# Optimization experiments

Measured on AMD Instinct MI355X. Metric: run time of the kernel, lower is better.

Reference implementation:

```python
import jax, jax.numpy as jnp
import numpy as np

N = 50000     # nodes
E = 400000    # nnz per hop matrix
K1 = 4        # K + 1 hops (K = 3)
D = 1280      # in_dim (pad_features target_dim)
H = 256       # hidden_dim


def setup_inputs() -> dict:
    key = jax.random.key(0)
    k0, k1, k2, k3, k4, k5 = jax.random.split(key, 6)
    X = jax.random.normal(k0, (N, D), dtype=jnp.float32)
    rows = jax.random.randint(k1, (K1, E), 0, N, dtype=jnp.int32)
    cols = jax.random.randint(k2, (K1, E), 0, N, dtype=jnp.int32)
    vals = jax.random.uniform(k3, (K1, E), dtype=jnp.float32)
    W = jax.random.normal(k4, (K1, D, H), dtype=jnp.float32) * 0.02
    b = jax.random.normal(k5, (K1, H), dtype=jnp.float32) * 0.02
    alpha = jnp.ones((1,), dtype=jnp.float32) * 0.25  # PReLU default init
    return {"X": X, "rows": rows, "cols": cols, "vals": vals,
            "W": W, "b": b, "alpha": alpha}


def _spmm(rows_k, cols_k, vals_k, X):
    # sparse A_k @ X: gather source rows, scale by edge values, scatter-add to dest rows
    return jax.ops.segment_sum(vals_k[:, None] * X[cols_k], rows_k, num_segments=N)


def reference(X, rows, cols, vals, W, b, alpha):
    out = jnp.zeros((N, H), dtype=X.dtype)
    for k in range(K1):  # small fixed hop count, structurally distinct matrices
        tmp = _spmm(rows[k], cols[k], vals[k], X)       # [N, D]
        out = out + tmp @ W[k] + b[k]                    # [N, H]
    # PReLU with single shared alpha
    return jnp.where(out >= 0, out, alpha * out)
```

## Files before the change

kernel.cpp:

```cpp
#include <hip/hip_runtime.h>
#include <hip/hip_bf16.h>
#include <stdint.h>

#define N_NODES 50000
#define E_EDGES 400000
#define K1H 4
#define D_IN 1280
#define H_OUT 256
#define NTOT 1024
#define MP 50176
#define MTILES 392
#define CAP 128

typedef float f32x4 __attribute__((ext_vector_type(4)));
typedef short s16x8 __attribute__((ext_vector_type(8)));

#define GLOBAL_AS __attribute__((address_space(1)))
#define LDS_AS __attribute__((address_space(3)))

__device__ __forceinline__ void g2lds16(const void* g, void* l) {
    __builtin_amdgcn_global_load_lds((const GLOBAL_AS uint32_t*)g,
                                     (LDS_AS uint32_t*)l, 16, 0, 0);
}

__device__ __forceinline__ ushort f2bf(float x) {
    uint32_t u = __float_as_uint(x);
    uint32_t r = u + 0x7FFFu + ((u >> 16) & 1u);
    return (ushort)(r >> 16);
}
__device__ __forceinline__ float bf2f(ushort u) {
    return __uint_as_float(((uint32_t)u) << 16);
}

__global__ void cvtX_kernel(const float* __restrict__ X, ushort* __restrict__ Xb) {
    int i = (blockIdx.x * 256 + threadIdx.x) * 4;
    ushort4 o;
    if (i < N_NODES * D_IN) {
        const float4 v = *(const float4*)(X + i);
        o.x = f2bf(v.x); o.y = f2bf(v.y); o.z = f2bf(v.z); o.w = f2bf(v.w);
    } else {
        o.x = 0; o.y = 0; o.z = 0; o.w = 0;
    }
    *(ushort4*)(Xb + i) = o;
}

__global__ void cvtW_kernel(const float* __restrict__ W, ushort* __restrict__ WbT) {
    int o = blockIdx.x * 256 + threadIdx.x;
    if (o >= NTOT * D_IN) return;
    int n = o / D_IN, d = o - n * D_IN;
    int k = n >> 8, h = n & 255;
    WbT[o] = f2bf(W[(k * D_IN + d) * H_OUT + h]);
}

__global__ void scatter_kernel(const int* __restrict__ rows, const int* __restrict__ cols,
                               const float* __restrict__ vals, int* __restrict__ cnt,
                               int2* __restrict__ edges) {
    int i = blockIdx.x * 256 + threadIdx.x;
    if (i >= K1H * E_EDGES) return;
    int k = i / E_EDGES;
    int r = rows[i];
    int pos = atomicAdd(&cnt[r], 1);
    if (pos < CAP)
        edges[(size_t)r * CAP + pos] =
            make_int2((cols[i] << 10) | (k << 8), __float_as_int(vals[i]));
}

__global__ void __launch_bounds__(256)
gemm_kernel(const ushort* __restrict__ Xb, const ushort* __restrict__ WbT,
            ushort* __restrict__ Yb) {
    __shared__ ushort lA[128 * 64];
    __shared__ ushort lB[128 * 64];
    const int bid = blockIdx.x;
    const int xcd = bid & 7, j = bid >> 3;
    const int rt = xcd + ((j >> 3) << 3);
    const int ct = j & 7;
    const int rowBase = rt * 128;
    const int colBase = ct * 128;
    const int t = threadIdx.x;
    const int w = t >> 6, lane = t & 63;
    const int quad = lane >> 4, l16 = lane & 15;
    const int wm = w >> 1, wn = w & 1;

    f32x4 acc[4][4] = {};

    int gaA[4], gaB[4];
    #pragma unroll
    for (int i = 0; i < 4; ++i) {
        const int c = t + 256 * i;
        const int row = c >> 3, kcs = (c & 7) ^ (row & 7);
        gaA[i] = (rowBase + row) * D_IN + kcs * 8;
        gaB[i] = (colBase + row) * D_IN + kcs * 8;
    }

    for (int kt = 0; kt < D_IN / 64; ++kt) {
        const int ko = kt * 64;
        #pragma unroll
        for (int i = 0; i < 4; ++i) {
            g2lds16(Xb + gaA[i] + ko, &lA[(t + 256 * i) * 8]);
            g2lds16(WbT + gaB[i] + ko, &lB[(t + 256 * i) * 8]);
        }
        __syncthreads();

        #pragma unroll
        for (int ks = 0; ks < 2; ++ks) {
            s16x8 af[4], bf[4];
            #pragma unroll
            for (int mt = 0; mt < 4; ++mt) {
                const int m = wm * 64 + mt * 16 + l16;
                af[mt] = *(const s16x8*)&lA[(m * 8 + ((ks * 4 + quad) ^ (m & 7))) * 8];
            }
            #pragma unroll
            for (int nt = 0; nt < 4; ++nt) {
                const int n = wn * 64 + nt * 16 + l16;
                bf[nt] = *(const s16x8*)&lB[(n * 8 + ((ks * 4 + quad) ^ (n & 7))) * 8];
            }
            #pragma unroll
            for (int mt = 0; mt < 4; ++mt)
                #pragma unroll
                for (int nt = 0; nt < 4; ++nt)
                    acc[mt][nt] = __builtin_amdgcn_mfma_f32_16x16x32_bf16(
                        af[mt], bf[nt], acc[mt][nt], 0, 0, 0);
        }
        __syncthreads();
    }

    #pragma unroll
    for (int mt = 0; mt < 4; ++mt) {
        #pragma unroll
        for (int nt = 0; nt < 4; ++nt) {
            const int rr = rowBase + wm * 64 + mt * 16 + quad * 4;
            const int cc = colBase + wn * 64 + nt * 16 + l16;
            #pragma unroll
            for (int r = 0; r < 4; ++r)
                Yb[(rr + r) * NTOT + cc] = f2bf(acc[mt][nt][r]);
        }
    }
}

__global__ void __launch_bounds__(256)
spmm_kernel(const int2* __restrict__ edges, const int* __restrict__ cnt,
            const ushort* __restrict__ Yb, const float* __restrict__ b,
            const float* __restrict__ alpha, float* __restrict__ out) {
    const int wid = threadIdx.x >> 6, lane = threadIdx.x & 63;
    const int row = blockIdx.x * 4 + wid;
    const int h0 = lane * 4;

    float4 acc = make_float4(0.f, 0.f, 0.f, 0.f);
    #pragma unroll
    for (int k = 0; k < K1H; ++k) {
        const float4 bb = *(const float4*)(b + k * H_OUT + h0);
        acc.x += bb.x; acc.y += bb.y; acc.z += bb.z; acc.w += bb.w;
    }

    const int2* eb = edges + (size_t)row * CAP;
    int e = cnt[row]; if (e > CAP) e = CAP;
    int j = 0;
    for (; j + 4 <= e; j += 4) {
        const int2 e0 = eb[j], e1 = eb[j + 1], e2 = eb[j + 2], e3 = eb[j + 3];
        const ushort4 y0 = *(const ushort4*)(Yb + e0.x + h0);
        const ushort4 y1 = *(const ushort4*)(Yb + e1.x + h0);
        const ushort4 y2 = *(const ushort4*)(Yb + e2.x + h0);
        const ushort4 y3 = *(const ushort4*)(Yb + e3.x + h0);
        const float v0 = __int_as_float(e0.y), v1 = __int_as_float(e1.y);
        const float v2 = __int_as_float(e2.y), v3 = __int_as_float(e3.y);
        acc.x += v0 * bf2f(y0.x) + v1 * bf2f(y1.x) + v2 * bf2f(y2.x) + v3 * bf2f(y3.x);
        acc.y += v0 * bf2f(y0.y) + v1 * bf2f(y1.y) + v2 * bf2f(y2.y) + v3 * bf2f(y3.y);
        acc.z += v0 * bf2f(y0.z) + v1 * bf2f(y1.z) + v2 * bf2f(y2.z) + v3 * bf2f(y3.z);
        acc.w += v0 * bf2f(y0.w) + v1 * bf2f(y1.w) + v2 * bf2f(y2.w) + v3 * bf2f(y3.w);
    }
    for (; j < e; ++j) {
        const int2 ed = eb[j];
        const float v = __int_as_float(ed.y);
        const ushort4 y = *(const ushort4*)(Yb + ed.x + h0);
        acc.x += v * bf2f(y.x);
        acc.y += v * bf2f(y.y);
        acc.z += v * bf2f(y.z);
        acc.w += v * bf2f(y.w);
    }

    const float a = alpha[0];
    float4 o;
    o.x = acc.x >= 0.f ? acc.x : a * acc.x;
    o.y = acc.y >= 0.f ? acc.y : a * acc.y;
    o.z = acc.z >= 0.f ? acc.z : a * acc.z;
    o.w = acc.w >= 0.f ? acc.w : a * acc.w;
    *(float4*)(out + row * H_OUT + h0) = o;
}

static inline size_t align256(size_t x) { return (x + 255) & ~(size_t)255; }

extern "C" void kernel_launch(void* const* d_in, const int* in_sizes, int n_in,
                              void* d_out, int out_size, void* d_ws, size_t ws_size,
                              hipStream_t stream) {
    const float* X     = (const float*)d_in[0];
    const int*   rows  = (const int*)d_in[1];
    const int*   cols  = (const int*)d_in[2];
    const float* vals  = (const float*)d_in[3];
    const float* W     = (const float*)d_in[4];
    const float* b     = (const float*)d_in[5];
    const float* alpha = (const float*)d_in[6];
    float* out = (float*)d_out;

    char* ws = (char*)d_ws;
    size_t off = 0;
    ushort* Xb  = (ushort*)(ws + off); off = align256(off + (size_t)MP * D_IN * 2);
    ushort* WbT = (ushort*)(ws + off); off = align256(off + (size_t)NTOT * D_IN * 2);
    ushort* Yb  = (ushort*)(ws + off); off = align256(off + (size_t)MP * NTOT * 2);
    int* cnt    = (int*)(ws + off);    off = align256(off + (size_t)N_NODES * 4);
    int2* edges = (int2*)(ws + off);   off = align256(off + (size_t)N_NODES * CAP * 8);

    hipMemsetAsync(cnt, 0, (size_t)N_NODES * 4, stream);

    cvtX_kernel<<<MP * D_IN / 4 / 256, 256, 0, stream>>>(X, Xb);
    cvtW_kernel<<<(NTOT * D_IN + 255) / 256, 256, 0, stream>>>(W, WbT);
    scatter_kernel<<<(K1H * E_EDGES + 255) / 256, 256, 0, stream>>>(rows, cols, vals, cnt, edges);
    gemm_kernel<<<MTILES * 8, 256, 0, stream>>>(Xb, WbT, Yb);
    spmm_kernel<<<N_NODES / 4, 256, 0, stream>>>(edges, cnt, Yb, b, alpha, out);
}
```

Measured before the change: 781.9 us.

## Rewrite GEMM as 256x256-tile, 8-wave, double-buffered LDS pipeline

Reworks the bf16 GEMM to use 256x256 output tiles computed by 512 threads, with double-buffered LDS and a hand-scheduled loop. The loop interleaves global-to-LDS staging of the next K slice with MFMA work on the current one, using explicit vmcnt/lgkmcnt waits, barriers and setprio. Larger tiles raise arithmetic intensity per byte loaded, and the overlap aims to hide load latency. In exchange it uses 128KB of LDS and many more registers, and the hand-written wait counts are fragile.

```diff
diff --git a/kernel.cpp b/kernel.cpp
--- a/kernel.cpp
+++ b/kernel.cpp
@@ -9,7 +9,6 @@
 #define H_OUT 256
 #define NTOT 1024
 #define MP 50176
-#define MTILES 392
 #define CAP 128
 
 typedef float f32x4 __attribute__((ext_vector_type(4)));
@@ -65,77 +64,124 @@
             make_int2((cols[i] << 10) | (k << 8), __float_as_int(vals[i]));
 }
 
-__global__ void __launch_bounds__(256)
+#define BARR() __builtin_amdgcn_s_barrier()
+#define LGKM0() { asm volatile("s_waitcnt lgkmcnt(0)" ::: "memory"); \
+                  __builtin_amdgcn_sched_barrier(0); }
+#define VMC(N) asm volatile("s_waitcnt vmcnt(" #N ")" ::: "memory")
+
+__global__ void __launch_bounds__(512, 2)
 gemm_kernel(const ushort* __restrict__ Xb, const ushort* __restrict__ WbT,
             ushort* __restrict__ Yb) {
-    __shared__ ushort lA[128 * 64];
-    __shared__ ushort lB[128 * 64];
+    __shared__ ushort lds[2][2][256 * 64];
+
     const int bid = blockIdx.x;
     const int xcd = bid & 7, j = bid >> 3;
-    const int rt = xcd + ((j >> 3) << 3);
-    const int ct = j & 7;
-    const int rowBase = rt * 128;
-    const int colBase = ct * 128;
+    const int j2 = xcd * 98 + j;
+    const int rt = j2 >> 2, ct = j2 & 3;
+    const int rowBase = rt * 256, colBase = ct * 256;
     const int t = threadIdx.x;
     const int w = t >> 6, lane = t & 63;
     const int quad = lane >> 4, l16 = lane & 15;
-    const int wm = w >> 1, wn = w & 1;
-
-    f32x4 acc[4][4] = {};
-
-    int gaA[4], gaB[4];
+    const int wm = w >> 2, wn = w & 3;
+
+    f32x4 acc[8][4] = {};
+    s16x8 af[4][2];
+    s16x8 bfr[2][2][2];
+
+    const int kcg = (t & 7) ^ ((t >> 3) & 7);
+    const ushort* pA = Xb + (rowBase + (t >> 3)) * D_IN + kcg * 8;
+    const ushort* pB = WbT + (colBase + (t >> 3) + wm * 32) * D_IN + kcg * 8;
+
+#define STAGE_A(BUF, G, KT) { _Pragma("unroll") \
+    for (int r = 0; r < 2; ++r) \
+        g2lds16(pA + (r * 128 + (G) * 64) * D_IN + (KT) * 64, \
+                &lds[BUF][0][(t + (G) * 512 + r * 1024) * 8]); }
+#define STAGE_B(BUF, G, KT) { _Pragma("unroll") \
+    for (int r = 0; r < 2; ++r) \
+        g2lds16(pB + (r * 128 + (G) * 32) * D_IN + (KT) * 64, \
+                &lds[BUF][1][(t + wm * 256 + (G) * 256 + r * 1024) * 8]); }
+#define LDA_F(BUF, MH) { _Pragma("unroll") \
+    for (int mt = 0; mt < 4; ++mt) { \
+        const int m = wm * 128 + (MH) * 64 + mt * 16 + l16; \
+        _Pragma("unroll") for (int ks = 0; ks < 2; ++ks) \
+            af[mt][ks] = *(const s16x8*)&lds[BUF][0][(m * 8 + ((ks * 4 + quad) ^ (l16 & 7))) * 8]; } }
+#define LDB_F(BUF, NH) { _Pragma("unroll") \
+    for (int nt = 0; nt < 2; ++nt) { \
+        const int n = wn * 64 + (NH) * 32 + nt * 16 + l16; \
+        _Pragma("unroll") for (int ks = 0; ks < 2; ++ks) \
+            bfr[NH][nt][ks] = *(const s16x8*)&lds[BUF][1][(n * 8 + ((ks * 4 + quad) ^ (l16 & 7))) * 8]; } }
+#define MMA_Q(MH, NH) { __builtin_amdgcn_s_setprio(1); \
+    _Pragma("unroll") for (int mt = 0; mt < 4; ++mt) \
+        _Pragma("unroll") for (int nt = 0; nt < 2; ++nt) \
+            _Pragma("unroll") for (int ks = 0; ks < 2; ++ks) \
+                acc[(MH) * 4 + mt][(NH) * 2 + nt] = \
+                    __builtin_amdgcn_mfma_f32_16x16x32_bf16(af[mt][ks], bfr[NH][nt][ks], \
+                        acc[(MH) * 4 + mt][(NH) * 2 + nt], 0, 0, 0); \
+    __builtin_amdgcn_s_setprio(0); }
+
+    STAGE_A(0, 0, 0); STAGE_B(0, 0, 0); STAGE_A(0, 1, 0); STAGE_B(0, 1, 0);
+    STAGE_A(1, 0, 1); STAGE_B(1, 0, 1);
+    VMC(8);
+    BARR();
+
+#pragma unroll 1
+    for (int i = 0; i < 9; ++i) {
+        const int kt0 = 2 * i;
+        LDA_F(0, 0); LDB_F(0, 0); STAGE_A(1, 1, kt0 + 1); VMC(6);
+        BARR(); LGKM0(); MMA_Q(0, 0); BARR();
+        LDB_F(0, 1); STAGE_B(1, 1, kt0 + 1);
+        BARR(); LGKM0(); MMA_Q(0, 1); BARR();
+        LDA_F(0, 1); STAGE_A(0, 0, kt0 + 2);
+        BARR(); LGKM0(); MMA_Q(1, 0); BARR();
+        STAGE_B(0, 0, kt0 + 2); VMC(8);
+        BARR(); MMA_Q(1, 1); BARR();
+        LDA_F(1, 0); LDB_F(1, 0); STAGE_A(0, 1, kt0 + 2); VMC(6);
+        BARR(); LGKM0(); MMA_Q(0, 0); BARR();
+        LDB_F(1, 1); STAGE_B(0, 1, kt0 + 2);
+        BARR(); LGKM0(); MMA_Q(0, 1); BARR();
+        LDA_F(1, 1); STAGE_A(1, 0, kt0 + 3);
+        BARR(); LGKM0(); MMA_Q(1, 0); BARR();
+        STAGE_B(1, 0, kt0 + 3); VMC(8);
+        BARR(); MMA_Q(1, 1); BARR();
+    }
+
+    LDA_F(0, 0); LDB_F(0, 0); STAGE_A(1, 1, 19); VMC(6);
+    BARR(); LGKM0(); MMA_Q(0, 0); BARR();
+    LDB_F(0, 1); STAGE_B(1, 1, 19);
+    BARR(); LGKM0(); MMA_Q(0, 1); BARR();
+    LDA_F(0, 1);
+    BARR(); LGKM0(); MMA_Q(1, 0); BARR();
+    VMC(4);
+    BARR(); MMA_Q(1, 1); BARR();
+    LDA_F(1, 0); LDB_F(1, 0); VMC(0);
+    BARR(); LGKM0(); MMA_Q(0, 0); BARR();
+    LDB_F(1, 1);
+    BARR(); LGKM0(); MMA_Q(0, 1); BARR();
+    LDA_F(1, 1);
+    BARR(); LGKM0(); MMA_Q(1, 0); BARR();
+    MMA_Q(1, 1);
+
     #pragma unroll
-    for (int i = 0; i < 4; ++i) {
-        const int c = t + 256 * i;
-        const int row = c >> 3, kcs = (c & 7) ^ (row & 7);
-        gaA[i] = (rowBase + row) * D_IN + kcs * 8;
-        gaB[i] = (colBase + row) * D_IN + kcs * 8;
-    }
-
-    for (int kt = 0; kt < D_IN / 64; ++kt) {
-        const int ko = kt * 64;
+    for (int mh = 0; mh < 2; ++mh)
+      #pragma unroll
+      for (int mt = 0; mt < 4; ++mt)
         #pragma unroll
-        for (int i = 0; i < 4; ++i) {
-            g2lds16(Xb + gaA[i] + ko, &lA[(t + 256 * i) * 8]);
-            g2lds16(WbT + gaB[i] + ko, &lB[(t + 256 * i) * 8]);
-        }
-        __syncthreads();
-
-        #pragma unroll
-        for (int ks = 0; ks < 2; ++ks) {
-            s16x8 af[4], bf[4];
-            #pragma unroll
-            for (int mt = 0; mt < 4; ++mt) {
-                const int m = wm * 64 + mt * 16 + l16;
-                af[mt] = *(const s16x8*)&lA[(m * 8 + ((ks * 4 + quad) ^ (m & 7))) * 8];
-            }
-            #pragma unroll
-            for (int nt = 0; nt < 4; ++nt) {
-                const int n = wn * 64 + nt * 16 + l16;
-                bf[nt] = *(const s16x8*)&lB[(n * 8 + ((ks * 4 + quad) ^ (n & 7))) * 8];
-            }
-            #pragma unroll
-            for (int mt = 0; mt < 4; ++mt)
-                #pragma unroll
-                for (int nt = 0; nt < 4; ++nt)
-                    acc[mt][nt] = __builtin_amdgcn_mfma_f32_16x16x32_bf16(
-                        af[mt], bf[nt], acc[mt][nt], 0, 0, 0);
-        }
-        __syncthreads();
-    }
-
-    #pragma unroll
-    for (int mt = 0; mt < 4; ++mt) {
-        #pragma unroll
-        for (int nt = 0; nt < 4; ++nt) {
-            const int rr = rowBase + wm * 64 + mt * 16 + quad * 4;
-            const int cc = colBase + wn * 64 + nt * 16 + l16;
+        for (int nh = 0; nh < 2; ++nh)
+          #pragma unroll
+          for (int nt = 0; nt < 2; ++nt) {
+            const int rr = rowBase + wm * 128 + mh * 64 + mt * 16 + quad * 4;
+            const int cc = colBase + wn * 64 + nh * 32 + nt * 16 + l16;
             #pragma unroll
             for (int r = 0; r < 4; ++r)
-                Yb[(rr + r) * NTOT + cc] = f2bf(acc[mt][nt][r]);
-        }
-    }
-}
+                Yb[(rr + r) * NTOT + cc] = f2bf(acc[mh * 4 + mt][nh * 2 + nt][r]);
+          }
+}
+
+#undef STAGE_A
+#undef STAGE_B
+#undef LDA_F
+#undef LDB_F
+#undef MMA_Q
 
 __global__ void __launch_bounds__(256)
 spmm_kernel(const int2* __restrict__ edges, const int* __restrict__ cnt,
@@ -214,6 +260,6 @@
     cvtX_kernel<<<MP * D_IN / 4 / 256, 256, 0, stream>>>(X, Xb);
     cvtW_kernel<<<(NTOT * D_IN + 255) / 256, 256, 0, stream>>>(W, WbT);
     scatter_kernel<<<(K1H * E_EDGES + 255) / 256, 256, 0, stream>>>(rows, cols, vals, cnt, edges);
-    gemm_kernel<<<MTILES * 8, 256, 0, stream>>>(Xb, WbT, Yb);
+    gemm_kernel<<<196 * 4, 512, 0, stream>>>(Xb, WbT, Yb);
     spmm_kernel<<<N_NODES / 4, 256, 0, stream>>>(edges, cnt, Yb, b, alpha, out);
 }
```

Result: faster. 750.4 us (-4.0%).
